# Kernel optimization log

Measured on AMD Instinct MI355X. Metric: run time of the kernel, lower is better.

The kernel has to match this reference:

```python
import jax, jax.numpy as jnp
import numpy as np

N = 12500      # nodes
E = 200000     # edges (avg degree 16)
IN = 32        # inp_dim
OUT = 32       # out_dim
ATTN = 32      # attn_rel_emb_dim
R = 200        # num_rels
NB = 50        # num_bases


def setup_inputs() -> dict:
    key = jax.random.key(0)
    ks = jax.random.split(key, 10)
    node_feat = jax.random.normal(ks[0], (N, IN), jnp.float32)
    total_edge = jax.random.randint(ks[1], (2, E), 0, N)
    total_target_relation = jax.random.normal(ks[2], (E, ATTN), jnp.float32)
    total_relation_embed = jax.random.normal(ks[3], (E, ATTN), jnp.float32)
    total_relation = jax.random.randint(ks[4], (E,), 0, R)
    # learned parameters (xavier-ish scale)
    weight = jax.random.normal(ks[5], (NB, IN, OUT), jnp.float32) * 0.1
    w_comp = jax.random.normal(ks[6], (R, NB), jnp.float32) * 0.1
    self_loop_weight = jax.random.normal(ks[7], (IN, OUT), jnp.float32) * 0.1
    A_w = jax.random.normal(ks[8], (IN, 2 * IN + 2 * ATTN), jnp.float32) * 0.1
    A_b = jnp.zeros((IN,), jnp.float32)
    B_w = jax.random.normal(ks[9], (1, IN), jnp.float32) * 0.1
    B_b = jnp.zeros((1,), jnp.float32)
    return {
        'node_feat': node_feat,
        'total_target_relation': total_target_relation,
        'total_relation_embed': total_relation_embed,
        'weight': weight,
        'w_comp': w_comp,
        'self_loop_weight': self_loop_weight,
        'A_w': A_w,
        'A_b': A_b,
        'B_w': B_w,
        'B_b': B_b,
        'total_edge': total_edge,
        'total_relation': total_relation,
    }


def reference(node_feat, total_target_relation, total_relation_embed,
              weight, w_comp, self_loop_weight, A_w, A_b, B_w, B_b,
              total_edge, total_relation):
    # basis decomposition: per-relation weight [R, IN, OUT]
    rel_w = jnp.einsum('rb,bio->rio', w_comp, weight)
    src = node_feat[total_edge[0]]            # [E, IN]
    tgt = node_feat[total_edge[1]]            # [E, IN]
    # per-edge relation-specific transform (bmm in torch)
    msg = jnp.einsum('ei,eio->eo', src, rel_w[total_relation])  # [E, OUT]
    curr = tgt @ self_loop_weight             # [E, OUT]
    # attention MLP: sigmoid(B(relu(A(concat))))
    e = jnp.concatenate([src, tgt, total_relation_embed, total_target_relation], axis=1)
    h = jax.nn.relu(e @ A_w.T + A_b)
    a = jax.nn.sigmoid(h @ B_w.T + B_b)       # [E, 1]
    curr = curr + msg * a
    # gnn_spmm(e2n_sp, curr): scatter-add edge messages to target nodes
    out = jax.ops.segment_sum(curr, total_edge[1], num_segments=node_feat.shape[0])
    return out  # [N, OUT]
```

## Files before the change

### kernel.cpp

```cpp
#include <hip/hip_runtime.h>

#define N_NODES 12500
#define N_EDGES 200000
#define DIM 32
#define N_REL 200
#define N_BASES 50

#define OUT_ELEMS   (N_NODES * DIM)
#define ZERO_BLOCKS ((OUT_ELEMS + 1023) / 1024)

#define PE_MAX 203008
#define N_DUMMY_BLOCKS 8

#define NB_BLK 200
#define CHUNK 1000

#define AWBF_OFF  (N_REL * 1024 * 2)
#define SLWT_OFF  (AWBF_OFF + 32 * 128 * 2)
#define BCT_OFF   (SLWT_OFF + 32 * 32 * 2)
#define BBT_OFF   (BCT_OFF + N_REL * NB_BLK * 4)
#define OFFS_OFF  (BBT_OFF + N_REL * NB_BLK * 4)
#define TOTS_OFF  (OFFS_OFF + 816)
#define SLOT_OFF  (TOTS_OFF + 800)

typedef __attribute__((ext_vector_type(8))) short short8;
typedef __attribute__((ext_vector_type(4))) float f32x4;

__device__ __forceinline__ unsigned short f2bf(float x) {
    union { float f; unsigned u; } v; v.f = x;
    unsigned r = (v.u + 0x7FFFu + ((v.u >> 16) & 1u)) >> 16;
    return (unsigned short)r;
}

__device__ __forceinline__ short8 cvt8(float4 a, float4 b) {
    short8 r;
    r[0] = (short)f2bf(a.x); r[1] = (short)f2bf(a.y);
    r[2] = (short)f2bf(a.z); r[3] = (short)f2bf(a.w);
    r[4] = (short)f2bf(b.x); r[5] = (short)f2bf(b.y);
    r[6] = (short)f2bf(b.z); r[7] = (short)f2bf(b.w);
    return r;
}

#define MFMA(A, B, C) __builtin_amdgcn_mfma_f32_16x16x32_bf16(A, B, C, 0, 0, 0)

__global__ __launch_bounds__(256) void prep_kernel(
    const float* __restrict__ weight,
    const float* __restrict__ w_comp,
    const float* __restrict__ Aw,
    const float* __restrict__ slw,
    const int*  __restrict__ rel,
    unsigned short* __restrict__ relwT_bf,
    unsigned short* __restrict__ aw_bf,
    unsigned short* __restrict__ slwT_bf,
    int* __restrict__ blockCountsT,
    float* __restrict__ out)
{
    int b = blockIdx.x, tid = threadIdx.x;
    if (b < N_REL) {
        __shared__ float wc[N_BASES];
        if (tid < N_BASES) wc[tid] = w_comp[b * N_BASES + tid];
        __syncthreads();
        const float* wp = weight + tid * 4;
        float4 acc = make_float4(0.f, 0.f, 0.f, 0.f);
        #pragma unroll 10
        for (int bb = 0; bb < N_BASES; bb++) {
            float4 w = *(const float4*)(wp + bb * 1024);
            float c = wc[bb];
            acc.x = fmaf(c, w.x, acc.x); acc.y = fmaf(c, w.y, acc.y);
            acc.z = fmaf(c, w.z, acc.z); acc.w = fmaf(c, w.w, acc.w);
        }
        int i  = tid >> 3;
        int o0 = (tid * 4) & 31;
        unsigned short* dst = relwT_bf + b * 1024 + i;
        dst[(o0 + 0) * 32] = f2bf(acc.x);
        dst[(o0 + 1) * 32] = f2bf(acc.y);
        dst[(o0 + 2) * 32] = f2bf(acc.z);
        dst[(o0 + 3) * 32] = f2bf(acc.w);
    } else if (b < N_REL + ZERO_BLOCKS) {
        int base = (b - N_REL) * 1024 + tid * 4;
        if (base + 3 < OUT_ELEMS)
            *(float4*)(out + base) = make_float4(0.f, 0.f, 0.f, 0.f);
        else
            for (int k = 0; k < 4; k++)
                if (base + k < OUT_ELEMS) out[base + k] = 0.f;
    } else if (b == N_REL + ZERO_BLOCKS) {
        for (int x = tid; x < 32 * 128; x += 256) aw_bf[x] = f2bf(Aw[x]);
        for (int x = tid; x < 32 * 32; x += 256) {
            int i = x >> 5, j = x & 31;
            slwT_bf[j * 32 + i] = f2bf(slw[x]);
        }
    } else {
        __shared__ int h[N_REL];
        int blk = b - (N_REL + ZERO_BLOCKS + 1);
        for (int x = tid; x < N_REL; x += 256) h[x] = 0;
        __syncthreads();
        int e0 = blk * CHUNK;
        for (int e = e0 + tid; e < e0 + CHUNK; e += 256) {
            int r = rel[e]; r = r < 0 ? 0 : (r >= N_REL ? N_REL - 1 : r);
            atomicAdd(&h[r], 1);
        }
        __syncthreads();
        for (int x = tid; x < N_REL; x += 256)
            blockCountsT[x * NB_BLK + blk] = h[x];
    }
}

__global__ __launch_bounds__(256) void scan_kernel(
    const int* __restrict__ blockCountsT,
    int* __restrict__ blockBaseT,
    int* __restrict__ offs, int* __restrict__ tots)
{
    __shared__ int s0[256];
    __shared__ int pval[256];
    int tid = threadIdx.x;
    int tot = 0;
    if (tid < N_REL) {
        const int4* cp = (const int4*)(blockCountsT + tid * NB_BLK);
        #pragma unroll 5
        for (int b = 0; b < NB_BLK / 4; b++) {
            int4 c = cp[b];
            tot += c.x + c.y + c.z + c.w;
        }
    }
    int p = (tid < N_REL) ? ((tot + 15) & ~15) : 0;
    pval[tid] = p;
    s0[tid] = p;
    __syncthreads();
    #pragma unroll
    for (int d = 1; d < 256; d <<= 1) {
        int v = s0[tid];
        if (tid >= d) v += s0[tid - d];
        __syncthreads();
        s0[tid] = v;
        __syncthreads();
    }
    int off = s0[tid] - pval[tid];
    if (tid < N_REL) { offs[tid] = off; tots[tid] = tot; }
    if (tid == 255) offs[N_REL] = s0[255];
    if (tid < N_REL) {
        const int4* cp = (const int4*)(blockCountsT + tid * NB_BLK);
        int4* bp = (int4*)(blockBaseT + tid * NB_BLK);
        int run = off;
        #pragma unroll 5
        for (int b = 0; b < NB_BLK / 4; b++) {
            int4 c = cp[b];
            int4 w;
            w.x = run;
            w.y = w.x + c.x;
            w.z = w.y + c.y;
            w.w = w.z + c.z;
            run = w.w + c.w;
            bp[b] = w;
        }
    }
}

__global__ __launch_bounds__(256) void scatter_kernel(
    const int* __restrict__ edge0, const int* __restrict__ edge1,
    const int* __restrict__ rel,
    const int* __restrict__ blockBaseT,
    const int* __restrict__ offs, const int* __restrict__ tots,
    int4* __restrict__ slot4)
{
    int blk = blockIdx.x, tid = threadIdx.x;
    if (blk < NB_BLK) {
        __shared__ int cur[N_REL];
        for (int x = tid; x < N_REL; x += 256)
            cur[x] = blockBaseT[x * NB_BLK + blk];
        __syncthreads();
        int e0 = blk * CHUNK;
        #pragma unroll
        for (int e = e0 + tid; e < e0 + CHUNK; e += 256) {
            int r = rel[e];   r = r < 0 ? 0 : (r >= N_REL   ? N_REL   - 1 : r);
            int s = edge0[e]; s = s < 0 ? 0 : (s >= N_NODES ? N_NODES - 1 : s);
            int t = edge1[e]; t = t < 0 ? 0 : (t >= N_NODES ? N_NODES - 1 : t);
            int pos = atomicAdd(&cur[r], 1);
            slot4[pos] = make_int4(s, t, e, r);
        }
    } else {
        int db = blk - NB_BLK;
        const int4 dummy = make_int4(0, -1, 0, 0);
        for (int r = db; r < N_REL; r += N_DUMMY_BLOCKS) {
            int start = offs[r] + tots[r];
            int end   = offs[r] + ((tots[r] + 15) & ~15);
            for (int j = start + tid; j < end; j += 256)
                slot4[j] = dummy;
        }
        int padTotal = offs[N_REL];
        for (int j = padTotal + db * 256 + tid; j < PE_MAX; j += N_DUMMY_BLOCKS * 256)
            slot4[j] = dummy;
    }
}

__global__ __launch_bounds__(256) void edge_kernel(
    const float* __restrict__ node_feat,
    const float* __restrict__ ttr,
    const float* __restrict__ tre,
    const float* __restrict__ Ab,
    const float* __restrict__ Bw,
    const float* __restrict__ Bb,
    const int4* __restrict__ slot4,
    const unsigned short* __restrict__ relwT_bf,
    const unsigned short* __restrict__ aw_bf,
    const unsigned short* __restrict__ slwT_bf,
    float* __restrict__ out)
{
    int tid  = threadIdx.x;
    int wave = tid >> 6;
    int lane = tid & 63;
    int m = lane & 15;
    int q = lane >> 4;
    int base = blockIdx.x * 64 + wave * 16;

    int s_ld = 0, t_ld = -1, e_ld = 0, r_ld = 0;
    if (lane < 16) {
        int4 v = slot4[base + lane];
        s_ld = v.x; t_ld = v.y; e_ld = v.z; r_ld = v.w;
    }
    int r_w = __shfl(r_ld, 0, 64);

    int s_m = __shfl(s_ld, m, 64);
    int t_m = __shfl(t_ld, m, 64);
    int e_m = __shfl(e_ld, m, 64);
    int t_mc = t_m < 0 ? 0 : t_m;

    const float* sp = node_feat + s_m * DIM + q * 8;
    float4 sv0 = *(const float4*)sp, sv1 = *(const float4*)(sp + 4);
    const float* tp = node_feat + t_mc * DIM + q * 8;
    float4 tv0 = *(const float4*)tp, tv1 = *(const float4*)(tp + 4);
    const float* rp = tre + e_m * DIM + q * 8;
    float4 rv0 = *(const float4*)rp, rv1 = *(const float4*)(rp + 4);
    const float* qp = ttr + e_m * DIM + q * 8;
    float4 qv0 = *(const float4*)qp, qv1 = *(const float4*)(qp + 4);

    short8 fsrc = cvt8(sv0, sv1);
    short8 ftgt = cvt8(tv0, tv1);
    short8 fre  = cvt8(rv0, rv1);
    short8 ftr  = cvt8(qv0, qv1);

    short8 bA[4][2], bS[2], bM[2];
    #pragma unroll
    for (int hh = 0; hh < 2; hh++) {
        #pragma unroll
        for (int c = 0; c < 4; c++)
            bA[c][hh] = *(const short8*)(aw_bf + (16 * hh + m) * 128 + 32 * c + 8 * q);
        bS[hh] = *(const short8*)(slwT_bf + (16 * hh + m) * 32 + 8 * q);
        bM[hh] = *(const short8*)(relwT_bf + r_w * 1024 + (16 * hh + m) * 32 + 8 * q);
    }

    float ab0 = Ab[m], ab1 = Ab[16 + m];
    f32x4 hacc0 = {ab0, ab0, ab0, ab0};
    f32x4 hacc1 = {ab1, ab1, ab1, ab1};
    f32x4 cacc0 = {0.f, 0.f, 0.f, 0.f};
    f32x4 cacc1 = {0.f, 0.f, 0.f, 0.f};
    f32x4 macc0 = {0.f, 0.f, 0.f, 0.f};
    f32x4 macc1 = {0.f, 0.f, 0.f, 0.f};

    hacc0 = MFMA(fsrc, bA[0][0], hacc0);  hacc1 = MFMA(fsrc, bA[0][1], hacc1);
    hacc0 = MFMA(ftgt, bA[1][0], hacc0);  hacc1 = MFMA(ftgt, bA[1][1], hacc1);
    hacc0 = MFMA(fre,  bA[2][0], hacc0);  hacc1 = MFMA(fre,  bA[2][1], hacc1);
    hacc0 = MFMA(ftr,  bA[3][0], hacc0);  hacc1 = MFMA(ftr,  bA[3][1], hacc1);
    cacc0 = MFMA(ftgt, bS[0], cacc0);     cacc1 = MFMA(ftgt, bS[1], cacc1);
    macc0 = MFMA(fsrc, bM[0], macc0);     macc1 = MFMA(fsrc, bM[1], macc1);

    float bw0 = Bw[m], bw1 = Bw[16 + m], Bb0 = Bb[0];
    float av[4];
    #pragma unroll
    for (int v = 0; v < 4; v++) {
        float p = fmaxf(hacc0[v], 0.f) * bw0 + fmaxf(hacc1[v], 0.f) * bw1;
        p += __shfl_xor(p, 1, 16);
        p += __shfl_xor(p, 2, 16);
        p += __shfl_xor(p, 4, 16);
        p += __shfl_xor(p, 8, 16);
        av[v] = 1.f / (1.f + __expf(-(p + Bb0)));
    }
    #pragma unroll
    for (int v = 0; v < 4; v++) {
        int row = 4 * q + v;
        int tv = __shfl(t_ld, row, 64);
        if (tv >= 0) {
            atomicAdd(&out[tv * DIM + m],      cacc0[v] + macc0[v] * av[v]);
            atomicAdd(&out[tv * DIM + 16 + m], cacc1[v] + macc1[v] * av[v]);
        }
    }
}

extern "C" void kernel_launch(void* const* d_in, const int* in_sizes, int n_in,
                              void* d_out, int out_size, void* d_ws, size_t ws_size,
                              hipStream_t stream) {
    const float* node_feat = (const float*)d_in[0];
    const float* ttr       = (const float*)d_in[1];
    const float* tre       = (const float*)d_in[2];
    const float* weight    = (const float*)d_in[3];
    const float* w_comp    = (const float*)d_in[4];
    const float* slw       = (const float*)d_in[5];
    const float* Aw        = (const float*)d_in[6];
    const float* Ab        = (const float*)d_in[7];
    const float* Bw        = (const float*)d_in[8];
    const float* Bb        = (const float*)d_in[9];
    const int*  total_edge = (const int*)d_in[10];
    const int*  rel        = (const int*)d_in[11];
    const int*  edge0 = total_edge;
    const int*  edge1 = total_edge + N_EDGES;

    char* ws = (char*)d_ws;
    unsigned short* relwT_bf = (unsigned short*)ws;
    unsigned short* aw_bf    = (unsigned short*)(ws + AWBF_OFF);
    unsigned short* slwT_bf  = (unsigned short*)(ws + SLWT_OFF);
    int*  blockCountsT = (int*)(ws + BCT_OFF);
    int*  blockBaseT   = (int*)(ws + BBT_OFF);
    int*  offs         = (int*)(ws + OFFS_OFF);
    int*  tots         = (int*)(ws + TOTS_OFF);
    int4* slot4        = (int4*)(ws + SLOT_OFF);
    float* out = (float*)d_out;

    prep_kernel<<<N_REL + ZERO_BLOCKS + 1 + NB_BLK, 256, 0, stream>>>(
        weight, w_comp, Aw, slw, rel, relwT_bf, aw_bf, slwT_bf,
        blockCountsT, out);

    scan_kernel<<<1, 256, 0, stream>>>(blockCountsT, blockBaseT, offs, tots);

    scatter_kernel<<<NB_BLK + N_DUMMY_BLOCKS, 256, 0, stream>>>(
        edge0, edge1, rel, blockBaseT, offs, tots, slot4);

    edge_kernel<<<PE_MAX / 64, 256, 0, stream>>>(
        node_feat, ttr, tre, Ab, Bw, Bb,
        slot4, relwT_bf, aw_bf, slwT_bf, out);
}
```

Before: 160.0 us.

## Compute attention gate in edge order and fold self-loop into per-node degree term

```diff
diff --git a/kernel.cpp b/kernel.cpp
--- a/kernel.cpp
+++ b/kernel.cpp
@@ -6,22 +6,24 @@
 #define N_REL 200
 #define N_BASES 50
 
-#define OUT_ELEMS   (N_NODES * DIM)
-#define ZERO_BLOCKS ((OUT_ELEMS + 1023) / 1024)
-
 #define PE_MAX 203008
 #define N_DUMMY_BLOCKS 8
 
 #define NB_BLK 200
 #define CHUNK 1000
 
+#define DEGZ_BLOCKS 13
+#define NODEOUT_BLOCKS 98
+#define GATE_BLOCKS 3125
+
 #define AWBF_OFF  (N_REL * 1024 * 2)
-#define SLWT_OFF  (AWBF_OFF + 32 * 128 * 2)
-#define BCT_OFF   (SLWT_OFF + 32 * 32 * 2)
+#define BCT_OFF   (AWBF_OFF + 32 * 128 * 2)
 #define BBT_OFF   (BCT_OFF + N_REL * NB_BLK * 4)
 #define OFFS_OFF  (BBT_OFF + N_REL * NB_BLK * 4)
 #define TOTS_OFF  (OFFS_OFF + 816)
-#define SLOT_OFF  (TOTS_OFF + 800)
+#define AGATE_OFF (TOTS_OFF + 800)
+#define DEG_OFF   (AGATE_OFF + N_EDGES * 4)
+#define SLOT_OFF  (DEG_OFF + 50000)
 
 typedef __attribute__((ext_vector_type(8))) short short8;
 typedef __attribute__((ext_vector_type(4))) float f32x4;
@@ -47,13 +49,11 @@
     const float* __restrict__ weight,
     const float* __restrict__ w_comp,
     const float* __restrict__ Aw,
-    const float* __restrict__ slw,
     const int*  __restrict__ rel,
     unsigned short* __restrict__ relwT_bf,
     unsigned short* __restrict__ aw_bf,
-    unsigned short* __restrict__ slwT_bf,
-    int* __restrict__ blockCountsT,
-    float* __restrict__ out)
+    int* __restrict__ deg,
+    int* __restrict__ blockCountsT)
 {
     int b = blockIdx.x, tid = threadIdx.x;
     if (b < N_REL) {
@@ -76,22 +76,15 @@
         dst[(o0 + 1) * 32] = f2bf(acc.y);
         dst[(o0 + 2) * 32] = f2bf(acc.z);
         dst[(o0 + 3) * 32] = f2bf(acc.w);
-    } else if (b < N_REL + ZERO_BLOCKS) {
-        int base = (b - N_REL) * 1024 + tid * 4;
-        if (base + 3 < OUT_ELEMS)
-            *(float4*)(out + base) = make_float4(0.f, 0.f, 0.f, 0.f);
-        else
-            for (int k = 0; k < 4; k++)
-                if (base + k < OUT_ELEMS) out[base + k] = 0.f;
-    } else if (b == N_REL + ZERO_BLOCKS) {
+    } else if (b == N_REL) {
         for (int x = tid; x < 32 * 128; x += 256) aw_bf[x] = f2bf(Aw[x]);
-        for (int x = tid; x < 32 * 32; x += 256) {
-            int i = x >> 5, j = x & 31;
-            slwT_bf[j * 32 + i] = f2bf(slw[x]);
-        }
+    } else if (b < N_REL + 1 + DEGZ_BLOCKS) {
+        int base = (b - (N_REL + 1)) * 1024 + tid * 4;
+        if (base < N_NODES)
+            *(int4*)(deg + base) = make_int4(0, 0, 0, 0);
     } else {
         __shared__ int h[N_REL];
-        int blk = b - (N_REL + ZERO_BLOCKS + 1);
+        int blk = b - (N_REL + 1 + DEGZ_BLOCKS);
         for (int x = tid; x < N_REL; x += 256) h[x] = 0;
         __syncthreads();
         int e0 = blk * CHUNK;
@@ -105,62 +98,138 @@
     }
 }
 
-__global__ __launch_bounds__(256) void scan_kernel(
+__global__ __launch_bounds__(256) void gate_scan_kernel(
+    const float* __restrict__ node_feat,
+    const float* __restrict__ ttr,
+    const float* __restrict__ tre,
+    const float* __restrict__ Ab,
+    const float* __restrict__ Bw,
+    const float* __restrict__ Bb,
+    const int*  __restrict__ edge0,
+    const int*  __restrict__ edge1,
+    const unsigned short* __restrict__ aw_bf,
     const int* __restrict__ blockCountsT,
     int* __restrict__ blockBaseT,
-    int* __restrict__ offs, int* __restrict__ tots)
+    int* __restrict__ offs, int* __restrict__ tots,
+    float* __restrict__ a_gate,
+    int* __restrict__ deg)
 {
-    __shared__ int s0[256];
-    __shared__ int pval[256];
-    int tid = threadIdx.x;
-    int tot = 0;
-    if (tid < N_REL) {
-        const int4* cp = (const int4*)(blockCountsT + tid * NB_BLK);
-        #pragma unroll 5
-        for (int b = 0; b < NB_BLK / 4; b++) {
-            int4 c = cp[b];
-            tot += c.x + c.y + c.z + c.w;
-        }
-    }
-    int p = (tid < N_REL) ? ((tot + 15) & ~15) : 0;
-    pval[tid] = p;
-    s0[tid] = p;
-    __syncthreads();
+    int b = blockIdx.x, tid = threadIdx.x;
+    if (b == GATE_BLOCKS) {
+        __shared__ int s0[256];
+        __shared__ int pval[256];
+        int tot = 0;
+        if (tid < N_REL) {
+            const int4* cp = (const int4*)(blockCountsT + tid * NB_BLK);
+            #pragma unroll 5
+            for (int bb = 0; bb < NB_BLK / 4; bb++) {
+                int4 c = cp[bb];
+                tot += c.x + c.y + c.z + c.w;
+            }
+        }
+        int p = (tid < N_REL) ? ((tot + 15) & ~15) : 0;
+        pval[tid] = p;
+        s0[tid] = p;
+        __syncthreads();
+        #pragma unroll
+        for (int d = 1; d < 256; d <<= 1) {
+            int v = s0[tid];
+            if (tid >= d) v += s0[tid - d];
+            __syncthreads();
+            s0[tid] = v;
+            __syncthreads();
+        }
+        int off = s0[tid] - pval[tid];
+        if (tid < N_REL) { offs[tid] = off; tots[tid] = tot; }
+        if (tid == 255) offs[N_REL] = s0[255];
+        if (tid < N_REL) {
+            const int4* cp = (const int4*)(blockCountsT + tid * NB_BLK);
+            int4* bp = (int4*)(blockBaseT + tid * NB_BLK);
+            int run = off;
+            #pragma unroll 5
+            for (int bb = 0; bb < NB_BLK / 4; bb++) {
+                int4 c = cp[bb];
+                int4 w;
+                w.x = run;
+                w.y = w.x + c.x;
+                w.z = w.y + c.y;
+                w.w = w.z + c.z;
+                run = w.w + c.w;
+                bp[bb] = w;
+            }
+        }
+        return;
+    }
+    int wave = tid >> 6;
+    int lane = tid & 63;
+    int m = lane & 15;
+    int q = lane >> 4;
+    int base = b * 64 + wave * 16;
+
+    int s_ld = 0, t_ld = 0;
+    if (lane < 16) {
+        int e = base + lane;
+        int s = edge0[e]; s_ld = s < 0 ? 0 : (s >= N_NODES ? N_NODES - 1 : s);
+        int t = edge1[e]; t_ld = t < 0 ? 0 : (t >= N_NODES ? N_NODES - 1 : t);
+        atomicAdd(&deg[t_ld], 1);
+    }
+    int s_m = __shfl(s_ld, m, 64);
+    int t_m = __shfl(t_ld, m, 64);
+    int e_m = base + m;
+
+    const float* sp = node_feat + s_m * DIM + q * 8;
+    float4 sv0 = *(const float4*)sp, sv1 = *(const float4*)(sp + 4);
+    const float* tp = node_feat + t_m * DIM + q * 8;
+    float4 tv0 = *(const float4*)tp, tv1 = *(const float4*)(tp + 4);
+    const float* rp = tre + e_m * DIM + q * 8;
+    float4 rv0 = *(const float4*)rp, rv1 = *(const float4*)(rp + 4);
+    const float* qp = ttr + e_m * DIM + q * 8;
+    float4 qv0 = *(const float4*)qp, qv1 = *(const float4*)(qp + 4);
+
+    short8 fsrc = cvt8(sv0, sv1);
+    short8 ftgt = cvt8(tv0, tv1);
+    short8 fre  = cvt8(rv0, rv1);
+    short8 ftr  = cvt8(qv0, qv1);
+
+    short8 bA[4][2];
     #pragma unroll
-    for (int d = 1; d < 256; d <<= 1) {
-        int v = s0[tid];
-        if (tid >= d) v += s0[tid - d];
-        __syncthreads();
-        s0[tid] = v;
-        __syncthreads();
-    }
-    int off = s0[tid] - pval[tid];
-    if (tid < N_REL) { offs[tid] = off; tots[tid] = tot; }
-    if (tid == 255) offs[N_REL] = s0[255];
-    if (tid < N_REL) {
-        const int4* cp = (const int4*)(blockCountsT + tid * NB_BLK);
-        int4* bp = (int4*)(blockBaseT + tid * NB_BLK);
-        int run = off;
-        #pragma unroll 5
-        for (int b = 0; b < NB_BLK / 4; b++) {
-            int4 c = cp[b];
-            int4 w;
-            w.x = run;
-            w.y = w.x + c.x;
-            w.z = w.y + c.y;
-            w.w = w.z + c.z;
-            run = w.w + c.w;
-            bp[b] = w;
-        }
-    }
-}
-
-__global__ __launch_bounds__(256) void scatter_kernel(
+    for (int hh = 0; hh < 2; hh++)
+        #pragma unroll
+        for (int c = 0; c < 4; c++)
+            bA[c][hh] = *(const short8*)(aw_bf + (16 * hh + m) * 128 + 32 * c + 8 * q);
+
+    float ab0 = Ab[m], ab1 = Ab[16 + m];
+    f32x4 hacc0 = {ab0, ab0, ab0, ab0};
+    f32x4 hacc1 = {ab1, ab1, ab1, ab1};
+    hacc0 = MFMA(fsrc, bA[0][0], hacc0);  hacc1 = MFMA(fsrc, bA[0][1], hacc1);
+    hacc0 = MFMA(ftgt, bA[1][0], hacc0);  hacc1 = MFMA(ftgt, bA[1][1], hacc1);
+    hacc0 = MFMA(fre,  bA[2][0], hacc0);  hacc1 = MFMA(fre,  bA[2][1], hacc1);
+    hacc0 = MFMA(ftr,  bA[3][0], hacc0);  hacc1 = MFMA(ftr,  bA[3][1], hacc1);
+
+    float bw0 = Bw[m], bw1 = Bw[16 + m], Bb0 = Bb[0];
+    #pragma unroll
+    for (int v = 0; v < 4; v++) {
+        float p = fmaxf(hacc0[v], 0.f) * bw0 + fmaxf(hacc1[v], 0.f) * bw1;
+        p += __shfl_xor(p, 1, 16);
+        p += __shfl_xor(p, 2, 16);
+        p += __shfl_xor(p, 4, 16);
+        p += __shfl_xor(p, 8, 16);
+        float a = 1.f / (1.f + __expf(-(p + Bb0)));
+        if (m == 0) a_gate[base + 4 * q + v] = a;
+    }
+}
+
+__global__ __launch_bounds__(256) void scatter_node_kernel(
     const int* __restrict__ edge0, const int* __restrict__ edge1,
     const int* __restrict__ rel,
     const int* __restrict__ blockBaseT,
     const int* __restrict__ offs, const int* __restrict__ tots,
-    int4* __restrict__ slot4)
+    const float* __restrict__ a_gate,
+    const float* __restrict__ node_feat,
+    const float* __restrict__ slw,
+    const int* __restrict__ deg,
+    int4* __restrict__ slot4,
+    float* __restrict__ out)
 {
     int blk = blockIdx.x, tid = threadIdx.x;
     if (blk < NB_BLK) {
@@ -169,15 +238,14 @@
             cur[x] = blockBaseT[x * NB_BLK + blk];
         __syncthreads();
         int e0 = blk * CHUNK;
-        #pragma unroll
         for (int e = e0 + tid; e < e0 + CHUNK; e += 256) {
             int r = rel[e];   r = r < 0 ? 0 : (r >= N_REL   ? N_REL   - 1 : r);
             int s = edge0[e]; s = s < 0 ? 0 : (s >= N_NODES ? N_NODES - 1 : s);
             int t = edge1[e]; t = t < 0 ? 0 : (t >= N_NODES ? N_NODES - 1 : t);
             int pos = atomicAdd(&cur[r], 1);
-            slot4[pos] = make_int4(s, t, e, r);
-        }
-    } else {
+            slot4[pos] = make_int4(s, t, __float_as_int(a_gate[e]), r);
+        }
+    } else if (blk < NB_BLK + N_DUMMY_BLOCKS) {
         int db = blk - NB_BLK;
         const int4 dummy = make_int4(0, -1, 0, 0);
         for (int r = db; r < N_REL; r += N_DUMMY_BLOCKS) {
@@ -189,20 +257,33 @@
         int padTotal = offs[N_REL];
         for (int j = padTotal + db * 256 + tid; j < PE_MAX; j += N_DUMMY_BLOCKS * 256)
             slot4[j] = dummy;
+    } else {
+        __shared__ float slws[32 * 32];
+        __shared__ float xs[8 * 32];
+        for (int x = tid; x < 32 * 32; x += 256) slws[x] = slw[x];
+        __syncthreads();
+        int n0 = (blk - (NB_BLK + N_DUMMY_BLOCKS)) * 128;
+        int rr = tid >> 5, j = tid & 31;
+        for (int pass = 0; pass < 16; pass++) {
+            int n = n0 + pass * 8 + rr;
+            xs[tid] = (n < N_NODES) ? node_feat[n * 32 + j] : 0.f;
+            __syncthreads();
+            if (n < N_NODES) {
+                float acc = 0.f;
+                #pragma unroll
+                for (int i = 0; i < 32; i++)
+                    acc = fmaf(xs[rr * 32 + i], slws[i * 32 + j], acc);
+                out[n * 32 + j] = (float)deg[n] * acc;
+            }
+            __syncthreads();
+        }
     }
 }
 
 __global__ __launch_bounds__(256) void edge_kernel(
     const float* __restrict__ node_feat,
-    const float* __restrict__ ttr,
-    const float* __restrict__ tre,
-    const float* __restrict__ Ab,
-    const float* __restrict__ Bw,
-    const float* __restrict__ Bb,
     const int4* __restrict__ slot4,
     const unsigned short* __restrict__ relwT_bf,
-    const unsigned short* __restrict__ aw_bf,
-    const unsigned short* __restrict__ slwT_bf,
     float* __restrict__ out)
 {
     int tid  = threadIdx.x;
@@ -212,75 +293,36 @@
     int q = lane >> 4;
     int base = blockIdx.x * 64 + wave * 16;
 
-    int s_ld = 0, t_ld = -1, e_ld = 0, r_ld = 0;
+    int s_ld = 0, t_ld = -1, a_ld = 0, r_ld = 0;
     if (lane < 16) {
         int4 v = slot4[base + lane];
-        s_ld = v.x; t_ld = v.y; e_ld = v.z; r_ld = v.w;
+        s_ld = v.x; t_ld = v.y; a_ld = v.z; r_ld = v.w;
     }
     int r_w = __shfl(r_ld, 0, 64);
-
     int s_m = __shfl(s_ld, m, 64);
-    int t_m = __shfl(t_ld, m, 64);
-    int e_m = __shfl(e_ld, m, 64);
-    int t_mc = t_m < 0 ? 0 : t_m;
 
     const float* sp = node_feat + s_m * DIM + q * 8;
     float4 sv0 = *(const float4*)sp, sv1 = *(const float4*)(sp + 4);
-    const float* tp = node_feat + t_mc * DIM + q * 8;
-    float4 tv0 = *(const float4*)tp, tv1 = *(const float4*)(tp + 4);
-    const float* rp = tre + e_m * DIM + q * 8;
-    float4 rv0 = *(const float4*)rp, rv1 = *(const float4*)(rp + 4);
-    const float* qp = ttr + e_m * DIM + q * 8;
-    float4 qv0 = *(const float4*)qp, qv1 = *(const float4*)(qp + 4);
-
     short8 fsrc = cvt8(sv0, sv1);
-    short8 ftgt = cvt8(tv0, tv1);
-    short8 fre  = cvt8(rv0, rv1);
-    short8 ftr  = cvt8(qv0, qv1);
-
-    short8 bA[4][2], bS[2], bM[2];
+
+    short8 bM[2];
     #pragma unroll
-    for (int hh = 0; hh < 2; hh++) {
-        #pragma unroll
-        for (int c = 0; c < 4; c++)
-            bA[c][hh] = *(const short8*)(aw_bf + (16 * hh + m) * 128 + 32 * c + 8 * q);
-        bS[hh] = *(const short8*)(slwT_bf + (16 * hh + m) * 32 + 8 * q);
+    for (int hh = 0; hh < 2; hh++)
         bM[hh] = *(const short8*)(relwT_bf + r_w * 1024 + (16 * hh + m) * 32 + 8 * q);
-    }
-
-    float ab0 = Ab[m], ab1 = Ab[16 + m];
-    f32x4 hacc0 = {ab0, ab0, ab0, ab0};
-    f32x4 hacc1 = {ab1, ab1, ab1, ab1};
-    f32x4 cacc0 = {0.f, 0.f, 0.f, 0.f};
-    f32x4 cacc1 = {0.f, 0.f, 0.f, 0.f};
+
     f32x4 macc0 = {0.f, 0.f, 0.f, 0.f};
     f32x4 macc1 = {0.f, 0.f, 0.f, 0.f};
-
-    hacc0 = MFMA(fsrc, bA[0][0], hacc0);  hacc1 = MFMA(fsrc, bA[0][1], hacc1);
-    hacc0 = MFMA(ftgt, bA[1][0], hacc0);  hacc1 = MFMA(ftgt, bA[1][1], hacc1);
-    hacc0 = MFMA(fre,  bA[2][0], hacc0);  hacc1 = MFMA(fre,  bA[2][1], hacc1);
-    hacc0 = MFMA(ftr,  bA[3][0], hacc0);  hacc1 = MFMA(ftr,  bA[3][1], hacc1);
-    cacc0 = MFMA(ftgt, bS[0], cacc0);     cacc1 = MFMA(ftgt, bS[1], cacc1);
-    macc0 = MFMA(fsrc, bM[0], macc0);     macc1 = MFMA(fsrc, bM[1], macc1);
-
-    float bw0 = Bw[m], bw1 = Bw[16 + m], Bb0 = Bb[0];
-    float av[4];
-    #pragma unroll
-    for (int v = 0; v < 4; v++) {
-        float p = fmaxf(hacc0[v], 0.f) * bw0 + fmaxf(hacc1[v], 0.f) * bw1;
-        p += __shfl_xor(p, 1, 16);
-        p += __shfl_xor(p, 2, 16);
-        p += __shfl_xor(p, 4, 16);
-        p += __shfl_xor(p, 8, 16);
-        av[v] = 1.f / (1.f + __expf(-(p + Bb0)));
-    }
+    macc0 = MFMA(fsrc, bM[0], macc0);
+    macc1 = MFMA(fsrc, bM[1], macc1);
+
     #pragma unroll
     for (int v = 0; v < 4; v++) {
         int row = 4 * q + v;
         int tv = __shfl(t_ld, row, 64);
+        float a_row = __int_as_float(__shfl(a_ld, row, 64));
         if (tv >= 0) {
-            atomicAdd(&out[tv * DIM + m],      cacc0[v] + macc0[v] * av[v]);
-            atomicAdd(&out[tv * DIM + 16 + m], cacc1[v] + macc1[v] * av[v]);
+            atomicAdd(&out[tv * DIM + m],      macc0[v] * a_row);
+            atomicAdd(&out[tv * DIM + 16 + m], macc1[v] * a_row);
         }
     }
 }
@@ -306,24 +348,26 @@
     char* ws = (char*)d_ws;
     unsigned short* relwT_bf = (unsigned short*)ws;
     unsigned short* aw_bf    = (unsigned short*)(ws + AWBF_OFF);
-    unsigned short* slwT_bf  = (unsigned short*)(ws + SLWT_OFF);
     int*  blockCountsT = (int*)(ws + BCT_OFF);
     int*  blockBaseT   = (int*)(ws + BBT_OFF);
     int*  offs         = (int*)(ws + OFFS_OFF);
     int*  tots         = (int*)(ws + TOTS_OFF);
+    float* a_gate      = (float*)(ws + AGATE_OFF);
+    int*  deg          = (int*)(ws + DEG_OFF);
     int4* slot4        = (int4*)(ws + SLOT_OFF);
     float* out = (float*)d_out;
 
-    prep_kernel<<<N_REL + ZERO_BLOCKS + 1 + NB_BLK, 256, 0, stream>>>(
-        weight, w_comp, Aw, slw, rel, relwT_bf, aw_bf, slwT_bf,
-        blockCountsT, out);
-
-    scan_kernel<<<1, 256, 0, stream>>>(blockCountsT, blockBaseT, offs, tots);
-
-    scatter_kernel<<<NB_BLK + N_DUMMY_BLOCKS, 256, 0, stream>>>(
-        edge0, edge1, rel, blockBaseT, offs, tots, slot4);
+    prep_kernel<<<N_REL + 1 + DEGZ_BLOCKS + NB_BLK, 256, 0, stream>>>(
+        weight, w_comp, Aw, rel, relwT_bf, aw_bf, deg, blockCountsT);
+
+    gate_scan_kernel<<<GATE_BLOCKS + 1, 256, 0, stream>>>(
+        node_feat, ttr, tre, Ab, Bw, Bb, edge0, edge1, aw_bf,
+        blockCountsT, blockBaseT, offs, tots, a_gate, deg);
+
+    scatter_node_kernel<<<NB_BLK + N_DUMMY_BLOCKS + NODEOUT_BLOCKS, 256, 0, stream>>>(
+        edge0, edge1, rel, blockBaseT, offs, tots, a_gate,
+        node_feat, slw, deg, slot4, out);
 
     edge_kernel<<<PE_MAX / 64, 256, 0, stream>>>(
-        node_feat, ttr, tre, Ab, Bw, Bb,
-        slot4, relwT_bf, aw_bf, slwT_bf, out);
-}
+        node_feat, slot4, relwT_bf, out);
+}
```

Result: slower. 177.7 us (+11.1%).

## Compute attention gate in edge order during bucket scatter, store gate in slot

Applied to the files above, without the earlier changes.

```diff
diff --git a/kernel.cpp b/kernel.cpp
--- a/kernel.cpp
+++ b/kernel.cpp
@@ -12,8 +12,12 @@
 #define PE_MAX 203008
 #define N_DUMMY_BLOCKS 8
 
-#define NB_BLK 200
-#define CHUNK 1000
+#define NB_BLK 196
+#define CHUNK 1024
+
+#define HIST_BASE (N_REL + 1 + ZERO_BLOCKS)
+#define PREP_BLOCKS (HIST_BASE + NB_BLK)
+#define EDGE_BLOCKS (PE_MAX / 256)
 
 #define AWBF_OFF  (N_REL * 1024 * 2)
 #define SLWT_OFF  (AWBF_OFF + 32 * 128 * 2)
@@ -76,26 +80,27 @@
         dst[(o0 + 1) * 32] = f2bf(acc.y);
         dst[(o0 + 2) * 32] = f2bf(acc.z);
         dst[(o0 + 3) * 32] = f2bf(acc.w);
-    } else if (b < N_REL + ZERO_BLOCKS) {
-        int base = (b - N_REL) * 1024 + tid * 4;
+    } else if (b == N_REL) {
+        for (int x = tid; x < 32 * 128; x += 256) aw_bf[x] = f2bf(Aw[x]);
+        for (int x = tid; x < 32 * 32; x += 256) {
+            int i = x >> 5, j = x & 31;
+            slwT_bf[j * 32 + i] = f2bf(slw[x]);
+        }
+    } else if (b < HIST_BASE) {
+        int base = (b - (N_REL + 1)) * 1024 + tid * 4;
         if (base + 3 < OUT_ELEMS)
             *(float4*)(out + base) = make_float4(0.f, 0.f, 0.f, 0.f);
         else
             for (int k = 0; k < 4; k++)
                 if (base + k < OUT_ELEMS) out[base + k] = 0.f;
-    } else if (b == N_REL + ZERO_BLOCKS) {
-        for (int x = tid; x < 32 * 128; x += 256) aw_bf[x] = f2bf(Aw[x]);
-        for (int x = tid; x < 32 * 32; x += 256) {
-            int i = x >> 5, j = x & 31;
-            slwT_bf[j * 32 + i] = f2bf(slw[x]);
-        }
     } else {
         __shared__ int h[N_REL];
-        int blk = b - (N_REL + ZERO_BLOCKS + 1);
+        int blk = b - HIST_BASE;
         for (int x = tid; x < N_REL; x += 256) h[x] = 0;
         __syncthreads();
         int e0 = blk * CHUNK;
-        for (int e = e0 + tid; e < e0 + CHUNK; e += 256) {
+        int e1 = e0 + CHUNK; if (e1 > N_EDGES) e1 = N_EDGES;
+        for (int e = e0 + tid; e < e1; e += 256) {
             int r = rel[e]; r = r < 0 ? 0 : (r >= N_REL ? N_REL - 1 : r);
             atomicAdd(&h[r], 1);
         }
@@ -116,7 +121,7 @@
     int tot = 0;
     if (tid < N_REL) {
         const int4* cp = (const int4*)(blockCountsT + tid * NB_BLK);
-        #pragma unroll 5
+        #pragma unroll 7
         for (int b = 0; b < NB_BLK / 4; b++) {
             int4 c = cp[b];
             tot += c.x + c.y + c.z + c.w;
@@ -141,7 +146,7 @@
         const int4* cp = (const int4*)(blockCountsT + tid * NB_BLK);
         int4* bp = (int4*)(blockBaseT + tid * NB_BLK);
         int run = off;
-        #pragma unroll 5
+        #pragma unroll 7
         for (int b = 0; b < NB_BLK / 4; b++) {
             int4 c = cp[b];
             int4 w;
@@ -155,30 +160,24 @@
     }
 }
 
-__global__ __launch_bounds__(256) void scatter_kernel(
-    const int* __restrict__ edge0, const int* __restrict__ edge1,
-    const int* __restrict__ rel,
+__global__ __launch_bounds__(256) void gatescatter_kernel(
+    const float* __restrict__ node_feat,
+    const float* __restrict__ ttr,
+    const float* __restrict__ tre,
+    const float* __restrict__ Ab,
+    const float* __restrict__ Bw,
+    const float* __restrict__ Bb,
+    const int*  __restrict__ edge0,
+    const int*  __restrict__ edge1,
+    const int*  __restrict__ rel,
+    const unsigned short* __restrict__ aw_bf,
     const int* __restrict__ blockBaseT,
     const int* __restrict__ offs, const int* __restrict__ tots,
     int4* __restrict__ slot4)
 {
-    int blk = blockIdx.x, tid = threadIdx.x;
-    if (blk < NB_BLK) {
-        __shared__ int cur[N_REL];
-        for (int x = tid; x < N_REL; x += 256)
-            cur[x] = blockBaseT[x * NB_BLK + blk];
-        __syncthreads();
-        int e0 = blk * CHUNK;
-        #pragma unroll
-        for (int e = e0 + tid; e < e0 + CHUNK; e += 256) {
-            int r = rel[e];   r = r < 0 ? 0 : (r >= N_REL   ? N_REL   - 1 : r);
-            int s = edge0[e]; s = s < 0 ? 0 : (s >= N_NODES ? N_NODES - 1 : s);
-            int t = edge1[e]; t = t < 0 ? 0 : (t >= N_NODES ? N_NODES - 1 : t);
-            int pos = atomicAdd(&cur[r], 1);
-            slot4[pos] = make_int4(s, t, e, r);
-        }
-    } else {
-        int db = blk - NB_BLK;
+    int b = blockIdx.x, tid = threadIdx.x;
+    if (b >= NB_BLK) {
+        int db = b - NB_BLK;
         const int4 dummy = make_int4(0, -1, 0, 0);
         for (int r = db; r < N_REL; r += N_DUMMY_BLOCKS) {
             int start = offs[r] + tots[r];
@@ -189,19 +188,96 @@
         int padTotal = offs[N_REL];
         for (int j = padTotal + db * 256 + tid; j < PE_MAX; j += N_DUMMY_BLOCKS * 256)
             slot4[j] = dummy;
+        return;
+    }
+
+    __shared__ int cur[N_REL];
+    for (int x = tid; x < N_REL; x += 256)
+        cur[x] = blockBaseT[x * NB_BLK + b];
+    __syncthreads();
+
+    int wave = tid >> 6;
+    int lane = tid & 63;
+    int m = lane & 15;
+    int q = lane >> 4;
+
+    short8 bA[4][2];
+    #pragma unroll
+    for (int hh = 0; hh < 2; hh++)
+        #pragma unroll
+        for (int c = 0; c < 4; c++)
+            bA[c][hh] = *(const short8*)(aw_bf + (16 * hh + m) * 128 + 32 * c + 8 * q);
+    float ab0 = Ab[m], ab1 = Ab[16 + m];
+    float bw0 = Bw[m], bw1 = Bw[16 + m], Bb0 = Bb[0];
+
+    int c0 = b * CHUNK;
+    int cend = c0 + CHUNK; if (cend > N_EDGES) cend = N_EDGES;
+    for (int it = 0; it < CHUNK / 256; it++) {
+        int ebase = c0 + it * 256 + wave * 64;
+        if (ebase >= cend) continue;
+
+        int e_lane = ebase + lane;
+        int s_ld = edge0[e_lane]; s_ld = s_ld < 0 ? 0 : (s_ld >= N_NODES ? N_NODES - 1 : s_ld);
+        int t_ld = edge1[e_lane]; t_ld = t_ld < 0 ? 0 : (t_ld >= N_NODES ? N_NODES - 1 : t_ld);
+        int r_ld = rel[e_lane];   r_ld = r_ld < 0 ? 0 : (r_ld >= N_REL   ? N_REL   - 1 : r_ld);
+
+        short8 fsrc[4], ftgt[4], fre_[4], ftr_[4];
+        #pragma unroll
+        for (int g = 0; g < 4; g++) {
+            int s_m = __shfl(s_ld, g * 16 + m, 64);
+            int t_m = __shfl(t_ld, g * 16 + m, 64);
+            int e_m = ebase + g * 16 + m;
+            const float* sp = node_feat + s_m * DIM + q * 8;
+            float4 sv0 = *(const float4*)sp, sv1 = *(const float4*)(sp + 4);
+            const float* tp = node_feat + t_m * DIM + q * 8;
+            float4 tv0 = *(const float4*)tp, tv1 = *(const float4*)(tp + 4);
+            const float* rp = tre + e_m * DIM + q * 8;
+            float4 rv0 = *(const float4*)rp, rv1 = *(const float4*)(rp + 4);
+            const float* qp = ttr + e_m * DIM + q * 8;
+            float4 qv0 = *(const float4*)qp, qv1 = *(const float4*)(qp + 4);
+            fsrc[g] = cvt8(sv0, sv1);
+            ftgt[g] = cvt8(tv0, tv1);
+            fre_[g] = cvt8(rv0, rv1);
+            ftr_[g] = cvt8(qv0, qv1);
+        }
+
+        #pragma unroll
+        for (int g = 0; g < 4; g++) {
+            f32x4 h0 = {ab0, ab0, ab0, ab0};
+            f32x4 h1 = {ab1, ab1, ab1, ab1};
+            h0 = MFMA(fsrc[g], bA[0][0], h0);  h1 = MFMA(fsrc[g], bA[0][1], h1);
+            h0 = MFMA(ftgt[g], bA[1][0], h0);  h1 = MFMA(ftgt[g], bA[1][1], h1);
+            h0 = MFMA(fre_[g], bA[2][0], h0);  h1 = MFMA(fre_[g], bA[2][1], h1);
+            h0 = MFMA(ftr_[g], bA[3][0], h0);  h1 = MFMA(ftr_[g], bA[3][1], h1);
+
+            float av[4];
+            #pragma unroll
+            for (int v = 0; v < 4; v++) {
+                float p = fmaxf(h0[v], 0.f) * bw0 + fmaxf(h1[v], 0.f) * bw1;
+                p += __shfl_xor(p, 1, 16);
+                p += __shfl_xor(p, 2, 16);
+                p += __shfl_xor(p, 4, 16);
+                p += __shfl_xor(p, 8, 16);
+                av[v] = 1.f / (1.f + __expf(-(p + Bb0)));
+            }
+            int j = g * 16 + 4 * q + m;
+            int s_j = __shfl(s_ld, j, 64);
+            int t_j = __shfl(t_ld, j, 64);
+            int r_j = __shfl(r_ld, j, 64);
+            float a_j = (m == 0) ? av[0] : (m == 1) ? av[1]
+                      : (m == 2) ? av[2] : av[3];
+            if (m < 4) {
+                int pos = atomicAdd(&cur[r_j], 1);
+                slot4[pos] = make_int4(s_j, t_j, __float_as_int(a_j), r_j);
+            }
+        }
     }
 }
 
 __global__ __launch_bounds__(256) void edge_kernel(
     const float* __restrict__ node_feat,
-    const float* __restrict__ ttr,
-    const float* __restrict__ tre,
-    const float* __restrict__ Ab,
-    const float* __restrict__ Bw,
-    const float* __restrict__ Bb,
     const int4* __restrict__ slot4,
     const unsigned short* __restrict__ relwT_bf,
-    const unsigned short* __restrict__ aw_bf,
     const unsigned short* __restrict__ slwT_bf,
     float* __restrict__ out)
 {
@@ -210,77 +286,51 @@
     int lane = tid & 63;
     int m = lane & 15;
     int q = lane >> 4;
-    int base = blockIdx.x * 64 + wave * 16;
-
-    int s_ld = 0, t_ld = -1, e_ld = 0, r_ld = 0;
-    if (lane < 16) {
-        int4 v = slot4[base + lane];
-        s_ld = v.x; t_ld = v.y; e_ld = v.z; r_ld = v.w;
-    }
-    int r_w = __shfl(r_ld, 0, 64);
-
-    int s_m = __shfl(s_ld, m, 64);
-    int t_m = __shfl(t_ld, m, 64);
-    int e_m = __shfl(e_ld, m, 64);
-    int t_mc = t_m < 0 ? 0 : t_m;
-
-    const float* sp = node_feat + s_m * DIM + q * 8;
-    float4 sv0 = *(const float4*)sp, sv1 = *(const float4*)(sp + 4);
-    const float* tp = node_feat + t_mc * DIM + q * 8;
-    float4 tv0 = *(const float4*)tp, tv1 = *(const float4*)(tp + 4);
-    const float* rp = tre + e_m * DIM + q * 8;
-    float4 rv0 = *(const float4*)rp, rv1 = *(const float4*)(rp + 4);
-    const float* qp = ttr + e_m * DIM + q * 8;
-    float4 qv0 = *(const float4*)qp, qv1 = *(const float4*)(qp + 4);
-
-    short8 fsrc = cvt8(sv0, sv1);
-    short8 ftgt = cvt8(tv0, tv1);
-    short8 fre  = cvt8(rv0, rv1);
-    short8 ftr  = cvt8(qv0, qv1);
-
-    short8 bA[4][2], bS[2], bM[2];
+    int wbase = blockIdx.x * 256 + wave * 64;
+
+    int4 v = slot4[wbase + lane];
+    int s_ld = v.x, t_ld = v.y, a_ld = v.z, r_ld = v.w;
+
+    short8 bS[2];
+    bS[0] = *(const short8*)(slwT_bf + m * 32 + 8 * q);
+    bS[1] = *(const short8*)(slwT_bf + (16 + m) * 32 + 8 * q);
+
+    short8 fsrc[4], ftgt[4], bM[4][2];
     #pragma unroll
-    for (int hh = 0; hh < 2; hh++) {
+    for (int g = 0; g < 4; g++) {
+        int r_g = __shfl(r_ld, g * 16, 64);
+        int s_m = __shfl(s_ld, g * 16 + m, 64);
+        int t_m = __shfl(t_ld, g * 16 + m, 64);
+        int t_mc = t_m < 0 ? 0 : t_m;
+        const float* sp = node_feat + s_m * DIM + q * 8;
+        float4 sv0 = *(const float4*)sp, sv1 = *(const float4*)(sp + 4);
+        const float* tp = node_feat + t_mc * DIM + q * 8;
+        float4 tv0 = *(const float4*)tp, tv1 = *(const float4*)(tp + 4);
+        fsrc[g] = cvt8(sv0, sv1);
+        ftgt[g] = cvt8(tv0, tv1);
+        bM[g][0] = *(const short8*)(relwT_bf + r_g * 1024 + m * 32 + 8 * q);
+        bM[g][1] = *(const short8*)(relwT_bf + r_g * 1024 + (16 + m) * 32 + 8 * q);
+    }
+
+    #pragma unroll
+    for (int g = 0; g < 4; g++) {
+        f32x4 m0 = {0.f, 0.f, 0.f, 0.f};
+        f32x4 m1 = {0.f, 0.f, 0.f, 0.f};
+        f32x4 c0 = {0.f, 0.f, 0.f, 0.f};
+        f32x4 c1 = {0.f, 0.f, 0.f, 0.f};
+        m0 = MFMA(fsrc[g], bM[g][0], m0);
+        m1 = MFMA(fsrc[g], bM[g][1], m1);
+        c0 = MFMA(ftgt[g], bS[0], c0);
+        c1 = MFMA(ftgt[g], bS[1], c1);
         #pragma unroll
-        for (int c = 0; c < 4; c++)
-            bA[c][hh] = *(const short8*)(aw_bf + (16 * hh + m) * 128 + 32 * c + 8 * q);
-        bS[hh] = *(const short8*)(slwT_bf + (16 * hh + m) * 32 + 8 * q);
-        bM[hh] = *(const short8*)(relwT_bf + r_w * 1024 + (16 * hh + m) * 32 + 8 * q);
-    }
-
-    float ab0 = Ab[m], ab1 = Ab[16 + m];
-    f32x4 hacc0 = {ab0, ab0, ab0, ab0};
-    f32x4 hacc1 = {ab1, ab1, ab1, ab1};
-    f32x4 cacc0 = {0.f, 0.f, 0.f, 0.f};
-    f32x4 cacc1 = {0.f, 0.f, 0.f, 0.f};
-    f32x4 macc0 = {0.f, 0.f, 0.f, 0.f};
-    f32x4 macc1 = {0.f, 0.f, 0.f, 0.f};
-
-    hacc0 = MFMA(fsrc, bA[0][0], hacc0);  hacc1 = MFMA(fsrc, bA[0][1], hacc1);
-    hacc0 = MFMA(ftgt, bA[1][0], hacc0);  hacc1 = MFMA(ftgt, bA[1][1], hacc1);
-    hacc0 = MFMA(fre,  bA[2][0], hacc0);  hacc1 = MFMA(fre,  bA[2][1], hacc1);
-    hacc0 = MFMA(ftr,  bA[3][0], hacc0);  hacc1 = MFMA(ftr,  bA[3][1], hacc1);
-    cacc0 = MFMA(ftgt, bS[0], cacc0);     cacc1 = MFMA(ftgt, bS[1], cacc1);
-    macc0 = MFMA(fsrc, bM[0], macc0);     macc1 = MFMA(fsrc, bM[1], macc1);
-
-    float bw0 = Bw[m], bw1 = Bw[16 + m], Bb0 = Bb[0];
-    float av[4];
-    #pragma unroll
-    for (int v = 0; v < 4; v++) {
-        float p = fmaxf(hacc0[v], 0.f) * bw0 + fmaxf(hacc1[v], 0.f) * bw1;
-        p += __shfl_xor(p, 1, 16);
-        p += __shfl_xor(p, 2, 16);
-        p += __shfl_xor(p, 4, 16);
-        p += __shfl_xor(p, 8, 16);
-        av[v] = 1.f / (1.f + __expf(-(p + Bb0)));
-    }
-    #pragma unroll
-    for (int v = 0; v < 4; v++) {
-        int row = 4 * q + v;
-        int tv = __shfl(t_ld, row, 64);
-        if (tv >= 0) {
-            atomicAdd(&out[tv * DIM + m],      cacc0[v] + macc0[v] * av[v]);
-            atomicAdd(&out[tv * DIM + 16 + m], cacc1[v] + macc1[v] * av[v]);
+        for (int vv = 0; vv < 4; vv++) {
+            int row = 4 * q + vv;
+            int tv = __shfl(t_ld, g * 16 + row, 64);
+            float a_row = __int_as_float(__shfl(a_ld, g * 16 + row, 64));
+            if (tv >= 0) {
+                atomicAdd(&out[tv * DIM + m],      c0[vv] + m0[vv] * a_row);
+                atomicAdd(&out[tv * DIM + 16 + m], c1[vv] + m1[vv] * a_row);
+            }
         }
     }
 }
@@ -314,16 +364,16 @@
     int4* slot4        = (int4*)(ws + SLOT_OFF);
     float* out = (float*)d_out;
 
-    prep_kernel<<<N_REL + ZERO_BLOCKS + 1 + NB_BLK, 256, 0, stream>>>(
+    prep_kernel<<<PREP_BLOCKS, 256, 0, stream>>>(
         weight, w_comp, Aw, slw, rel, relwT_bf, aw_bf, slwT_bf,
         blockCountsT, out);
 
     scan_kernel<<<1, 256, 0, stream>>>(blockCountsT, blockBaseT, offs, tots);
 
-    scatter_kernel<<<NB_BLK + N_DUMMY_BLOCKS, 256, 0, stream>>>(
-        edge0, edge1, rel, blockBaseT, offs, tots, slot4);
-
-    edge_kernel<<<PE_MAX / 64, 256, 0, stream>>>(
-        node_feat, ttr, tre, Ab, Bw, Bb,
-        slot4, relwT_bf, aw_bf, slwT_bf, out);
-}
+    gatescatter_kernel<<<NB_BLK + N_DUMMY_BLOCKS, 256, 0, stream>>>(
+        node_feat, ttr, tre, Ab, Bw, Bb, edge0, edge1, rel,
+        aw_bf, blockBaseT, offs, tots, slot4);
+
+    edge_kernel<<<EDGE_BLOCKS, 256, 0, stream>>>(
+        node_feat, slot4, relwT_bf, slwT_bf, out);
+}
```

After: 172.3 us. 1.08x slower.
